# Optimization experiments

Hardware: AMD Instinct MI355X
Metric: run time of the kernel (lower is better)

Reference implementation:

```python
import jax, jax.numpy as jnp
import numpy as np

SIZE = 512
HEADS = 4
DK = SIZE // HEADS
CHUNK = 16
SHIFT = 8
EPS = 1e-12


def layer_norm(x, g, b):
    m = jnp.mean(x, axis=-1, keepdims=True)
    v = jnp.var(x, axis=-1, keepdims=True)
    return (x - m) / jnp.sqrt(v + EPS) * g + b


def setup_inputs() -> dict:
    key = jax.random.key(0)
    ks = jax.random.split(key, 8)
    B, L, C = 16, 2048, SIZE
    p = lambda k, shp: jax.random.normal(k, shp, jnp.float32) * 0.02
    return {
        "x": jax.random.normal(ks[0], (B, L, C), jnp.float32),
        "mask": jnp.ones((B, 1, L), jnp.float32),
        "pos_emb": jnp.zeros((1, L, C), jnp.float32),
        "mask_pad": jnp.ones((B, 1, L), jnp.float32),
        "Wq": p(ks[1], (C, C)), "bq": jnp.zeros((C,), jnp.float32),
        "Wk": p(ks[2], (C, C)), "bk": jnp.zeros((C,), jnp.float32),
        "Wv": p(ks[3], (C, C)), "bv": jnp.zeros((C,), jnp.float32),
        "Wo": p(ks[4], (C, C)), "bo": jnp.zeros((C,), jnp.float32),
        "g1": jnp.ones((C,), jnp.float32), "be1": jnp.zeros((C,), jnp.float32),
        "g2": jnp.ones((C,), jnp.float32), "be2": jnp.zeros((C,), jnp.float32),
        "W1": p(ks[5], (C, 4 * C)), "bf1": jnp.zeros((4 * C,), jnp.float32),
        "W2": p(ks[6], (4 * C, C)), "bf2": jnp.zeros((C,), jnp.float32),
    }


def reference(x, mask, pos_emb, mask_pad, Wq, bq, Wk, bk, Wv, bv, Wo, bo,
              g1, be1, g2, be2, W1, bf1, W2, bf2):
    B, L, C = x.shape
    nW = L // CHUNK
    half = CHUNK // 2
    # shifted-window attention mask, built exactly as in the torch code
    # (zeros base, -100 in the cross-shift blocks); shape (nW, CHUNK, CHUNK)
    am = jnp.zeros((nW, CHUNK, CHUNK), x.dtype)
    am = am.at[:-1, :half - 1, half:].set(-100.0)
    am = am.at[-1, half:, half:].set(-100.0)

    residual = x
    xn = layer_norm(x, g1, be1)  # normalize_before

    # cyclic shift
    sx = jnp.roll(xn, -SHIFT, axis=1)                    # (B, L, C)
    sm = jnp.roll(mask_pad[:, 0, :], -SHIFT, axis=1)     # (B, L)

    # chunk partition
    xc = sx.reshape(B, nW, CHUNK, C)
    mc = sm.reshape(B, nW, CHUNK)

    # windowed multi-head attention
    q = (xc @ Wq + bq).reshape(B, nW, CHUNK, HEADS, DK)
    k = (xc @ Wk + bk).reshape(B, nW, CHUNK, HEADS, DK)
    v = (xc @ Wv + bv).reshape(B, nW, CHUNK, HEADS, DK)
    scores = jnp.einsum('bwqhd,bwkhd->bwhqk', q, k) / jnp.sqrt(jnp.asarray(DK, x.dtype))
    scores = scores + am[None, :, None]                  # add shift mask per chunk
    valid = mc[:, :, None, None, :] > 0.0                # key padding mask
    scores = jnp.where(valid, scores, jnp.asarray(-1e30, x.dtype))
    attn = jax.nn.softmax(scores, axis=-1)
    attn = jnp.where(valid, attn, jnp.asarray(0.0, x.dtype))
    out = jnp.einsum('bwhqk,bwkhd->bwqhd', attn, v).reshape(B, nW, CHUNK, C)
    out = out @ Wo + bo

    # chunk reverse + reverse shift
    sx_out = out.reshape(B, L, C)
    xa = jnp.roll(sx_out, SHIFT, axis=1)
    m = jnp.roll(sm, SHIFT, axis=1)
    xa = xa * m[:, :, None]
    x1 = residual + xa  # dropout_rate = 0

    # feed forward block (pre-norm, ReLU FFN)
    residual2 = x1
    xn2 = layer_norm(x1, g2, be2)
    h = jax.nn.relu(xn2 @ W1 + bf1)
    x2 = residual2 + (h @ W2 + bf2)
    return x2
```

## Files before the change

kernel.cpp:

```cpp
#include <hip/hip_runtime.h>
#include <stdint.h>


typedef unsigned short bfu;

using bf16x8 = __attribute__((ext_vector_type(8))) __bf16;
using f32x4  = __attribute__((ext_vector_type(4))) float;

union U8 { uint4 v; unsigned short s[8]; };
union F4 { float4 v; float f[4]; };
union ABFrag { uint4 u; bf16x8 f; };

__device__ __forceinline__ float bf2f(unsigned short u) {
    union { uint32_t i; float f; } c; c.i = ((uint32_t)u) << 16; return c.f;
}
__device__ __forceinline__ unsigned short f2bf(float f) {
    union { float f; uint32_t i; } c; c.f = f;
    uint32_t x = c.i;
    return (unsigned short)((x + 0x7FFFu + ((x >> 16) & 1u)) >> 16);
}
__device__ __forceinline__ uint4 pack8(float4 a, float4 b) {
    U8 o;
    o.s[0] = f2bf(a.x); o.s[1] = f2bf(a.y); o.s[2] = f2bf(a.z); o.s[3] = f2bf(a.w);
    o.s[4] = f2bf(b.x); o.s[5] = f2bf(b.y); o.s[6] = f2bf(b.z); o.s[7] = f2bf(b.w);
    return o.v;
}

#define GLDS16(gp, lp)                                                        \
    __builtin_amdgcn_global_load_lds(                                         \
        (__attribute__((address_space(1))) void*)(gp),                        \
        (__attribute__((address_space(3))) void*)(lp), 16, 0, 0)


__global__ __launch_bounds__(256) void wconv_kernel(
    const float* __restrict__ W, bfu* __restrict__ Wt, int K, int N)
{
    __shared__ float t[32][33];
    const int bn = blockIdx.x << 5;
    const int bk = blockIdx.y << 5;
    const int tx = threadIdx.x & 31, ty = threadIdx.x >> 5;
#pragma unroll
    for (int i = 0; i < 32; i += 8)
        t[ty + i][tx] = W[(size_t)(bk + ty + i) * N + bn + tx];
    __syncthreads();
#pragma unroll
    for (int i = 0; i < 32; i += 8)
        Wt[(size_t)(bn + ty + i) * K + bk + tx] = f2bf(t[tx][ty + i]);
}

__global__ __launch_bounds__(256) void bias_concat_kernel(
    const float* __restrict__ a, const float* __restrict__ b,
    const float* __restrict__ c, float* __restrict__ o)
{
    const int t = blockIdx.x * 256 + threadIdx.x;
    const float* src = (t < 512) ? a : (t < 1024) ? b : c;
    o[t] = src[t & 511];
}


__global__ __launch_bounds__(64) void ln1_shift_kernel(
    const float* __restrict__ x, const float* __restrict__ g,
    const float* __restrict__ be, bfu* __restrict__ out)
{
    const int ms = blockIdx.x;
    const int b = ms >> 11;
    const int ls = ms & 2047;
    const int l = (ls + 8) & 2047;
    const int c0 = threadIdx.x << 3;
    const float* xp = x + ((((size_t)(b << 11)) + l) << 9) + c0;
    F4 f0, f1; f0.v = *(const float4*)xp; f1.v = *(const float4*)(xp + 4);
    float vv[8]; float s = 0.f, sq = 0.f;
#pragma unroll
    for (int j = 0; j < 4; ++j) { vv[j] = f0.f[j]; vv[4 + j] = f1.f[j]; }
#pragma unroll
    for (int j = 0; j < 8; ++j) { s += vv[j]; sq += vv[j] * vv[j]; }
#pragma unroll
    for (int o = 32; o > 0; o >>= 1) { s += __shfl_xor(s, o); sq += __shfl_xor(sq, o); }
    const float mean = s * (1.f / 512.f);
    float var = sq * (1.f / 512.f) - mean * mean;
    var = fmaxf(var, 0.f);
    const float rstd = rsqrtf(var + 1e-12f);
    F4 g0, g1v, b0, b1;
    g0.v = *(const float4*)(g + c0);  g1v.v = *(const float4*)(g + c0 + 4);
    b0.v = *(const float4*)(be + c0); b1.v = *(const float4*)(be + c0 + 4);
    U8 o8;
#pragma unroll
    for (int j = 0; j < 4; ++j) {
        o8.s[j]     = f2bf((vv[j]     - mean) * rstd * g0.f[j]  + b0.f[j]);
        o8.s[4 + j] = f2bf((vv[4 + j] - mean) * rstd * g1v.f[j] + b1.f[j]);
    }
    *(uint4*)(out + (((size_t)ms) << 9) + c0) = o8.v;
}

__global__ __launch_bounds__(64) void ln2_kernel(
    const bfu* __restrict__ x1, const float* __restrict__ g,
    const float* __restrict__ be, bfu* __restrict__ out)
{
    const int ms = blockIdx.x;
    const int c0 = threadIdx.x << 3;
    U8 u; u.v = *(const uint4*)(x1 + (((size_t)ms) << 9) + c0);
    float vv[8]; float s = 0.f, sq = 0.f;
#pragma unroll
    for (int j = 0; j < 8; ++j) { float f = bf2f(u.s[j]); vv[j] = f; s += f; sq += f * f; }
#pragma unroll
    for (int o = 32; o > 0; o >>= 1) { s += __shfl_xor(s, o); sq += __shfl_xor(sq, o); }
    const float mean = s * (1.f / 512.f);
    float var = sq * (1.f / 512.f) - mean * mean;
    var = fmaxf(var, 0.f);
    const float rstd = rsqrtf(var + 1e-12f);
    F4 g0, g1v, b0, b1;
    g0.v = *(const float4*)(g + c0);  g1v.v = *(const float4*)(g + c0 + 4);
    b0.v = *(const float4*)(be + c0); b1.v = *(const float4*)(be + c0 + 4);
    U8 o8;
#pragma unroll
    for (int j = 0; j < 4; ++j) {
        o8.s[j]     = f2bf((vv[j]     - mean) * rstd * g0.f[j]  + b0.f[j]);
        o8.s[4 + j] = f2bf((vv[4 + j] - mean) * rstd * g1v.f[j] + b1.f[j]);
    }
    *(uint4*)(out + (((size_t)ms) << 9) + c0) = o8.v;
}


template<int EPI>
__global__ __launch_bounds__(512, 2) void mgemm(
    const bfu* __restrict__ X, const bfu* __restrict__ Wt,
    const float* __restrict__ bias,
    bfu* Ob, float* Ofl,
    const float* __restrict__ xres, const bfu* __restrict__ prevb,
    const float* __restrict__ maskpad,
    int M, int N, int K)
{
    __shared__ __align__(16) char smem[131072];
    bfu* smb = (bfu*)smem;
    const char* smc = (const char*)smem;
    float* epi = (float*)smem;

    const int t = threadIdx.x;
    const int lane = t & 63;
    const int w = t >> 6;
    const int wm = w >> 2, wn = w & 3;
    const int q = lane >> 4, l15 = lane & 15;

    const int gx = gridDim.x;
    const int nwg = gx * gridDim.y;
    int wid = blockIdx.y * gx + blockIdx.x;
    wid = ((wid & 7) * (nwg >> 3)) + (wid >> 3);
    const int row0 = (wid / gx) << 8;
    const int col0 = (wid % gx) << 8;

    const int srow = (w << 3) + (lane >> 3);
    const int scol = (((lane & 7) ^ ((lane >> 3) & 7)) << 3);
    const bfu* gA = X  + (size_t)(row0 + srow) * K + scol;
    const bfu* gB = Wt + (size_t)(col0 + srow) * K + scol;
    bfu* lsA0 = smb + (w << 9) + (lane << 3);
    bfu* lsB0 = lsA0 + 16384;
    bfu* lsA1 = lsA0 + 32768;
    bfu* lsB1 = lsA0 + 49152;

    const int arow = ((wm << 7) + l15) << 7;
    const int brow = ((wn << 6) + l15) << 7;
    const int qb   = q << 4;
    const int swz  = (l15 & 7) << 4;

    f32x4 acc[8][4];
    float bv[4];
#pragma unroll
    for (int j = 0; j < 4; ++j) bv[j] = bias[col0 + (wn << 6) + (j << 4) + l15];
#pragma unroll
    for (int i = 0; i < 8; ++i)
#pragma unroll
        for (int j = 0; j < 4; ++j) {
            acc[i][j][0] = bv[j]; acc[i][j][1] = bv[j];
            acc[i][j][2] = bv[j]; acc[i][j][3] = bv[j];
        }

    ABFrag a[4][2];
    ABFrag bb[2][2][2];

#define SB_   __builtin_amdgcn_s_barrier()
#define VM8_  asm volatile("s_waitcnt vmcnt(8)" ::: "memory")
#define VM0_  asm volatile("s_waitcnt vmcnt(0)" ::: "memory")
#define VMNOP_ do {} while (0)

#define LDA_(D, MH)                                                           \
    _Pragma("unroll") for (int mf = 0; mf < 4; ++mf)                          \
    _Pragma("unroll") for (int kk = 0; kk < 2; ++kk)                          \
        a[mf][kk].u = *(const uint4*)(smc + (D)*65536 + arow + (MH)*8192 +    \
                                      mf*2048 + (((kk << 6) + qb) ^ swz));
#define LDB_(D, NH)                                                           \
    _Pragma("unroll") for (int nf = 0; nf < 2; ++nf)                          \
    _Pragma("unroll") for (int kk = 0; kk < 2; ++kk)                          \
        bb[NH][nf][kk].u = *(const uint4*)(smc + (D)*65536 + 32768 + brow +   \
                                      (NH)*4096 + nf*2048 +                   \
                                      (((kk << 6) + qb) ^ swz));
#define MFMAQ_(MH, NH)                                                        \
    __builtin_amdgcn_s_setprio(1);                                            \
    _Pragma("unroll") for (int mf = 0; mf < 4; ++mf)                          \
    _Pragma("unroll") for (int nf = 0; nf < 2; ++nf) {                        \
        acc[(MH)*4+mf][(NH)*2+nf] = __builtin_amdgcn_mfma_f32_16x16x32_bf16(  \
            a[mf][0].f, bb[NH][nf][0].f, acc[(MH)*4+mf][(NH)*2+nf], 0, 0, 0); \
        acc[(MH)*4+mf][(NH)*2+nf] = __builtin_amdgcn_mfma_f32_16x16x32_bf16(  \
            a[mf][1].f, bb[NH][nf][1].f, acc[(MH)*4+mf][(NH)*2+nf], 0, 0, 0);}\
    __builtin_amdgcn_s_setprio(0);
#define STGA4_(D, GA2) do {                                                   \
    GLDS16((GA2), lsA##D);                                                    \
    GLDS16((GA2) + (size_t)64  * K, lsA##D + 4096);                           \
    GLDS16((GA2) + (size_t)128 * K, lsA##D + 8192);                           \
    GLDS16((GA2) + (size_t)192 * K, lsA##D + 12288); } while (0)
#define STGB4_(D, GB2) do {                                                   \
    GLDS16((GB2), lsB##D);                                                    \
    GLDS16((GB2) + (size_t)64  * K, lsB##D + 4096);                           \
    GLDS16((GB2) + (size_t)128 * K, lsB##D + 8192);                           \
    GLDS16((GB2) + (size_t)192 * K, lsB##D + 12288); } while (0)
#define TILE_(D, DOSTG, VMW) do {                                             \
    SB_;                                                                      \
    LDA_(D, 0); LDB_(D, 0);                                                   \
    MFMAQ_(0, 0);                                                             \
    SB_;                                                                      \
    LDB_(D, 1);                                                               \
    MFMAQ_(0, 1);                                                             \
    SB_;                                                                      \
    LDA_(D, 1);                                                               \
    if (DOSTG) STGB4_(D, gB2);                                                \
    MFMAQ_(1, 0);                                                             \
    SB_;                                                                      \
    if (DOSTG) STGA4_(D, gA2);                                                \
    MFMAQ_(1, 1);                                                             \
    VMW;                                                                      \
} while (0)

    const int nT = K >> 6;

    STGA4_(0, gA); STGB4_(0, gB);
    {
        const bfu* ga1 = gA + 64; const bfu* gb1 = gB + 64;
        STGA4_(1, ga1); STGB4_(1, gb1);
    }
    VM8_;

    const bfu* gA2 = gA + 128;
    const bfu* gB2 = gB + 128;
#pragma unroll 1
    for (int tt = 0; tt < nT - 2; tt += 2) {
        TILE_(0, true, VM8_);
        gA2 += 64; gB2 += 64;
        TILE_(1, true, VM8_);
        gA2 += 64; gB2 += 64;
    }
    TILE_(0, false, VM0_);
    TILE_(1, false, VMNOP_);

#undef LDA_
#undef LDB_
#undef MFMAQ_
#undef STGA4_
#undef STGB4_
#undef TILE_

    SB_;

    float* epw = epi + w * 1088;
    const int c8 = (lane & 7) << 3;
    const int r8 = lane >> 3;
    const int colg = col0 + (wn << 6) + c8;
#pragma unroll
    for (int i = 0; i < 8; ++i) {
#pragma unroll
        for (int j = 0; j < 4; ++j)
#pragma unroll
            for (int r = 0; r < 4; ++r) {
                float y = acc[i][j][r];
                if (EPI == 1) y = fmaxf(y, 0.f);
                epw[((q << 2) + r) * 68 + (j << 4) + l15] = y;
            }
        __builtin_amdgcn_wave_barrier();
#pragma unroll
        for (int h = 0; h < 2; ++h) {
            const int rr = r8 + (h << 3);
            F4 f0, f1;
            f0.v = *(const float4*)&epw[rr * 68 + c8];
            f1.v = *(const float4*)&epw[rr * 68 + c8 + 4];
            const int row_out = row0 + (wm << 7) + (i << 4) + rr;
            if (EPI == 0 || EPI == 1) {
                *(uint4*)(Ob + (size_t)row_out * N + colg) = pack8(f0.v, f1.v);
            } else if (EPI == 2) {
                const int bb2 = row_out >> 11;
                const int ls = row_out & 2047;
                const int l = (ls + 8) & 2047;
                const float mp = maskpad[(bb2 << 11) + l];
                const size_t dst = ((size_t)(bb2 << 11) + l) * (size_t)N + colg;
                F4 x0, x1v;
                x0.v = *(const float4*)(xres + dst);
                x1v.v = *(const float4*)(xres + dst + 4);
                F4 o0, o1;
#pragma unroll
                for (int jj = 0; jj < 4; ++jj) {
                    o0.f[jj] = x0.f[jj]  + f0.f[jj] * mp;
                    o1.f[jj] = x1v.f[jj] + f1.f[jj] * mp;
                }
                *(uint4*)(Ob + dst) = pack8(o0.v, o1.v);
            } else {
                const size_t dst = (size_t)row_out * N + colg;
                U8 pb; pb.v = *(const uint4*)(prevb + dst);
                F4 o0, o1;
#pragma unroll
                for (int jj = 0; jj < 4; ++jj) {
                    o0.f[jj] = bf2f(pb.s[jj])     + f0.f[jj];
                    o1.f[jj] = bf2f(pb.s[4 + jj]) + f1.f[jj];
                }
                *(float4*)(Ofl + dst) = o0.v;
                *(float4*)(Ofl + dst + 4) = o1.v;
            }
        }
        __builtin_amdgcn_wave_barrier();
    }
}


__global__ __launch_bounds__(256) void attn_kernel(
    const bfu* __restrict__ qkv, const float* __restrict__ mpad,
    bfu* __restrict__ out)
{
    __shared__ float qs[16][144];
    __shared__ float ks[16][144];
    __shared__ float vs[16][144];
    __shared__ float ps[16][17];
    const int t = threadIdx.x;
    const int wg = blockIdx.x;
    const int h = blockIdx.y;
    const int b = wg >> 7;
    const int w = wg & 127;
    const int li = t >> 4;
    const int d0 = (t & 15) << 3;
    const size_t bi = (((size_t)wg << 4) + li) * 1536 + (h << 7) + d0;
    U8 uq, uk, uv;
    uq.v = *(const uint4*)(qkv + bi);
    uk.v = *(const uint4*)(qkv + bi + 512);
    uv.v = *(const uint4*)(qkv + bi + 1024);
    F4 a0, a1;
#pragma unroll
    for (int j = 0; j < 4; ++j) { a0.f[j] = bf2f(uq.s[j]); a1.f[j] = bf2f(uq.s[4 + j]); }
    *(float4*)&qs[li][d0] = a0.v;  *(float4*)&qs[li][d0 + 4] = a1.v;
#pragma unroll
    for (int j = 0; j < 4; ++j) { a0.f[j] = bf2f(uk.s[j]); a1.f[j] = bf2f(uk.s[4 + j]); }
    *(float4*)&ks[li][d0] = a0.v;  *(float4*)&ks[li][d0 + 4] = a1.v;
#pragma unroll
    for (int j = 0; j < 4; ++j) { a0.f[j] = bf2f(uv.s[j]); a1.f[j] = bf2f(uv.s[4 + j]); }
    *(float4*)&vs[li][d0] = a0.v;  *(float4*)&vs[li][d0 + 4] = a1.v;
    __syncthreads();
    const int qi = li, ki = t & 15;
    float s = 0.f;
#pragma unroll
    for (int d = 0; d < 128; d += 4) {
        F4 qv, kv;
        qv.v = *(const float4*)&qs[qi][d];
        kv.v = *(const float4*)&ks[ki][d];
        s += qv.f[0] * kv.f[0] + qv.f[1] * kv.f[1]
           + qv.f[2] * kv.f[2] + qv.f[3] * kv.f[3];
    }
    s *= 0.088388347648318447f;
    const bool lastw = (w == 127);
    if (lastw ? (qi >= 8 && ki >= 8) : (qi < 7 && ki >= 8)) s -= 100.f;
    const int lkey = ((w << 4) + ki + 8) & 2047;
    const bool valid = mpad[(b << 11) + lkey] > 0.f;
    if (!valid) s = -1e30f;
    float mx = s;
#pragma unroll
    for (int o = 8; o > 0; o >>= 1) mx = fmaxf(mx, __shfl_xor(mx, o, 16));
    float e = __expf(s - mx);
    float sum = e;
#pragma unroll
    for (int o = 8; o > 0; o >>= 1) sum += __shfl_xor(sum, o, 16);
    float p = e / sum;
    if (!valid) p = 0.f;
    ps[qi][ki] = p;
    __syncthreads();
    F4 o0, o1;
#pragma unroll
    for (int j = 0; j < 4; ++j) { o0.f[j] = 0.f; o1.f[j] = 0.f; }
#pragma unroll
    for (int kk = 0; kk < 16; ++kk) {
        const float pw = ps[li][kk];
        F4 v0, v1;
        v0.v = *(const float4*)&vs[kk][d0];
        v1.v = *(const float4*)&vs[kk][d0 + 4];
#pragma unroll
        for (int j = 0; j < 4; ++j) {
            o0.f[j] += pw * v0.f[j];
            o1.f[j] += pw * v1.f[j];
        }
    }
    U8 o8;
#pragma unroll
    for (int j = 0; j < 4; ++j) { o8.s[j] = f2bf(o0.f[j]); o8.s[4 + j] = f2bf(o1.f[j]); }
    *(uint4*)(out + (((size_t)wg << 4) + li) * 512 + (h << 7) + d0) = o8.v;
}


extern "C" void kernel_launch(void* const* d_in, const int* in_sizes, int n_in,
                              void* d_out, int out_size, void* d_ws, size_t ws_size,
                              hipStream_t stream)
{
    const float* x    = (const float*)d_in[0];
    const float* mpad = (const float*)d_in[3];
    const float* Wq = (const float*)d_in[4];  const float* bq = (const float*)d_in[5];
    const float* Wk = (const float*)d_in[6];  const float* bk = (const float*)d_in[7];
    const float* Wv = (const float*)d_in[8];  const float* bv = (const float*)d_in[9];
    const float* Wo = (const float*)d_in[10]; const float* bo = (const float*)d_in[11];
    const float* g1 = (const float*)d_in[12]; const float* be1 = (const float*)d_in[13];
    const float* g2 = (const float*)d_in[14]; const float* be2 = (const float*)d_in[15];
    const float* W1 = (const float*)d_in[16]; const float* bf1 = (const float*)d_in[17];
    const float* W2 = (const float*)d_in[18]; const float* bf2 = (const float*)d_in[19];
    float* out = (float*)d_out;

    char* p = (char*)d_ws;
    const size_t MB = (size_t)1 << 20;
    bfu* xn_s = (bfu*)p;
    bfu* att  = xn_s;
    bfu* qkv  = (bfu*)(p + 32 * MB);
    bfu* x1   = qkv;
    bfu* W1t  = (bfu*)(p + 64 * MB);
    bfu* W2t  = (bfu*)(p + 66 * MB);
    bfu* xn2  = (bfu*)(p + 96 * MB);
    bfu* hreg = (bfu*)(p + 128 * MB);
    bfu* Wqkvt = hreg;
    bfu* Wot   = hreg + 1536 * 512;
    float* bqkv = (float*)(hreg + 2048 * 512);

    const int M = 32768;
    dim3 blk(256);
    dim3 blk5(512);

    wconv_kernel<<<dim3(16, 16), blk, 0, stream>>>(Wq, Wqkvt, 512, 512);
    wconv_kernel<<<dim3(16, 16), blk, 0, stream>>>(Wk, Wqkvt + 512 * 512, 512, 512);
    wconv_kernel<<<dim3(16, 16), blk, 0, stream>>>(Wv, Wqkvt + 1024 * 512, 512, 512);
    wconv_kernel<<<dim3(16, 16), blk, 0, stream>>>(Wo, Wot, 512, 512);
    bias_concat_kernel<<<dim3(6), blk, 0, stream>>>(bq, bk, bv, bqkv);

    ln1_shift_kernel<<<32768, 64, 0, stream>>>(x, g1, be1, xn_s);

    mgemm<0><<<dim3(6, 128), blk5, 0, stream>>>(xn_s, Wqkvt, bqkv, qkv, nullptr, nullptr, nullptr, nullptr, M, 1536, 512);

    attn_kernel<<<dim3(2048, 4), blk, 0, stream>>>(qkv, mpad, att);

    wconv_kernel<<<dim3(64, 16), blk, 0, stream>>>(W1, W1t, 512, 2048);
    wconv_kernel<<<dim3(16, 64), blk, 0, stream>>>(W2, W2t, 2048, 512);

    mgemm<2><<<dim3(2, 128), blk5, 0, stream>>>(att, Wot, bo, x1, nullptr, x, nullptr, mpad, M, 512, 512);

    ln2_kernel<<<32768, 64, 0, stream>>>(x1, g2, be2, xn2);

    mgemm<1><<<dim3(8, 128), blk5, 0, stream>>>(xn2, W1t, bf1, hreg, nullptr, nullptr, nullptr, nullptr, M, 2048, 512);
    mgemm<3><<<dim3(2, 128), blk5, 0, stream>>>(hreg, W2t, bf2, nullptr, out, nullptr, x1, nullptr, M, 512, 2048);
}
```

Before: 511.3 us.

## Prefetch next tile's B fragments during last MFMA quarter and merge QKV weight conversion

Restructures the GEMM main loop so the first B-fragment LDS reads for the next K tile are issued before the last MFMA quarter of the current tile. The vmcnt wait moves earlier with a tighter count, plus an extra barrier, so the next buffer is ready. This hides LDS read latency at the tile boundary but adds a barrier and a stricter wait on outstanding global-to-LDS loads. Separately, the three Q/K/V weight transpose-convert launches are merged into one 3D-grid launch to cut launch overhead.

```diff
diff --git a/kernel.cpp b/kernel.cpp
--- a/kernel.cpp
+++ b/kernel.cpp
@@ -46,6 +46,26 @@
 #pragma unroll
     for (int i = 0; i < 32; i += 8)
         Wt[(size_t)(bn + ty + i) * K + bk + tx] = f2bf(t[tx][ty + i]);
+}
+
+__global__ __launch_bounds__(256) void wconv3_kernel(
+    const float* __restrict__ Wq, const float* __restrict__ Wk,
+    const float* __restrict__ Wv, bfu* __restrict__ Wt)
+{
+    __shared__ float t[32][33];
+    const int z = blockIdx.z;
+    const float* W = (z == 0) ? Wq : (z == 1) ? Wk : Wv;
+    bfu* Wo = Wt + (size_t)z * 512 * 512;
+    const int bn = blockIdx.x << 5;
+    const int bk = blockIdx.y << 5;
+    const int tx = threadIdx.x & 31, ty = threadIdx.x >> 5;
+#pragma unroll
+    for (int i = 0; i < 32; i += 8)
+        t[ty + i][tx] = W[(size_t)(bk + ty + i) * 512 + bn + tx];
+    __syncthreads();
+#pragma unroll
+    for (int i = 0; i < 32; i += 8)
+        Wo[(size_t)(bn + ty + i) * 512 + bk + tx] = f2bf(t[tx][ty + i]);
 }
 
 __global__ __launch_bounds__(256) void bias_concat_kernel(
@@ -179,6 +199,7 @@
 
 #define SB_   __builtin_amdgcn_s_barrier()
 #define VM8_  asm volatile("s_waitcnt vmcnt(8)" ::: "memory")
+#define VM4_  asm volatile("s_waitcnt vmcnt(4)" ::: "memory")
 #define VM0_  asm volatile("s_waitcnt vmcnt(0)" ::: "memory")
 #define VMNOP_ do {} while (0)
 
@@ -212,9 +233,9 @@
     GLDS16((GB2) + (size_t)64  * K, lsB##D + 4096);                           \
     GLDS16((GB2) + (size_t)128 * K, lsB##D + 8192);                           \
     GLDS16((GB2) + (size_t)192 * K, lsB##D + 12288); } while (0)
-#define TILE_(D, DOSTG, VMW) do {                                             \
+#define TILE_(D, DOSTG, LASTT, VMW) do {                                      \
     SB_;                                                                      \
-    LDA_(D, 0); LDB_(D, 0);                                                   \
+    LDA_(D, 0);                                                               \
     MFMAQ_(0, 0);                                                             \
     SB_;                                                                      \
     LDB_(D, 1);                                                               \
@@ -224,9 +245,11 @@
     if (DOSTG) STGB4_(D, gB2);                                                \
     MFMAQ_(1, 0);                                                             \
     SB_;                                                                      \
+    VMW;                                                                      \
+    SB_;                                                                      \
+    if (!(LASTT)) LDB_((D)^1, 0);                                             \
     if (DOSTG) STGA4_(D, gA2);                                                \
     MFMAQ_(1, 1);                                                             \
-    VMW;                                                                      \
 } while (0)
 
     const int nT = K >> 6;
@@ -237,18 +260,20 @@
         STGA4_(1, ga1); STGB4_(1, gb1);
     }
     VM8_;
+    SB_;
+    LDB_(0, 0);
 
     const bfu* gA2 = gA + 128;
     const bfu* gB2 = gB + 128;
 #pragma unroll 1
     for (int tt = 0; tt < nT - 2; tt += 2) {
-        TILE_(0, true, VM8_);
+        TILE_(0, true, false, VM4_);
         gA2 += 64; gB2 += 64;
-        TILE_(1, true, VM8_);
+        TILE_(1, true, false, VM4_);
         gA2 += 64; gB2 += 64;
     }
-    TILE_(0, false, VM0_);
-    TILE_(1, false, VMNOP_);
+    TILE_(0, false, false, VM0_);
+    TILE_(1, false, true,  VMNOP_);
 
 #undef LDA_
 #undef LDB_
@@ -431,9 +456,7 @@
     dim3 blk(256);
     dim3 blk5(512);
 
-    wconv_kernel<<<dim3(16, 16), blk, 0, stream>>>(Wq, Wqkvt, 512, 512);
-    wconv_kernel<<<dim3(16, 16), blk, 0, stream>>>(Wk, Wqkvt + 512 * 512, 512, 512);
-    wconv_kernel<<<dim3(16, 16), blk, 0, stream>>>(Wv, Wqkvt + 1024 * 512, 512, 512);
+    wconv3_kernel<<<dim3(16, 16, 3), blk, 0, stream>>>(Wq, Wk, Wv, Wqkvt);
     wconv_kernel<<<dim3(16, 16), blk, 0, stream>>>(Wo, Wot, 512, 512);
     bias_concat_kernel<<<dim3(6), blk, 0, stream>>>(bq, bk, bv, bqkv);
 
```

Measured after the change: 558.1 us. 9.2% more time.
